# Optimization experiments

Hardware: AMD Instinct MI355X
Metric: run time of the kernel (lower is better)

The kernel has to match this reference:

```python
import jax, jax.numpy as jnp
import numpy as np

HIDDEN = 256
HEADS = 8
HEAD_DIM = HIDDEN // HEADS
NUM_RBF = 32
CUTOFF = 8.0
K_PTS = 4096   # total points (32 molecules x 128)
N_ATOMS = 2048 # total atoms  (32 molecules x 64)
B_MOL = 32


def setup_inputs() -> dict:
    key = jax.random.key(0)
    ks = jax.random.split(key, 12)
    s = 0.02
    return {
        "h_point": jax.random.normal(ks[0], (K_PTS, HIDDEN), jnp.float32),
        "h_atom": jax.random.normal(ks[1], (N_ATOMS, HIDDEN), jnp.float32),
        "pos_point": jax.random.uniform(ks[2], (K_PTS, 3), jnp.float32) * 10.0,
        "pos_atom": jax.random.uniform(ks[3], (N_ATOMS, 3), jnp.float32) * 10.0,
        "Wq": jax.random.normal(ks[4], (HIDDEN, HIDDEN), jnp.float32) * s,
        "bq": jnp.zeros((HIDDEN,), jnp.float32),
        "Wk": jax.random.normal(ks[5], (HIDDEN, HIDDEN), jnp.float32) * s,
        "bk": jnp.zeros((HIDDEN,), jnp.float32),
        "Wv": jax.random.normal(ks[6], (HIDDEN, HIDDEN), jnp.float32) * s,
        "bv": jnp.zeros((HIDDEN,), jnp.float32),
        "Wo": jax.random.normal(ks[7], (HIDDEN, HIDDEN), jnp.float32) * s,
        "bo": jnp.zeros((HIDDEN,), jnp.float32),
        "W_rbf": jax.random.normal(ks[8], (NUM_RBF, HEADS), jnp.float32) * 0.1,
        "b_rbf": jnp.zeros((HEADS,), jnp.float32),
        "centers": jnp.linspace(0.0, CUTOFF, NUM_RBF, dtype=jnp.float32),
        "gamma": jnp.ones((HIDDEN,), jnp.float32),
        "beta": jnp.zeros((HIDDEN,), jnp.float32),
        "point_batch": jnp.repeat(jnp.arange(B_MOL), K_PTS // B_MOL),
        "atom_batch": jnp.repeat(jnp.arange(B_MOL), N_ATOMS // B_MOL),
    }


def reference(h_point, h_atom, pos_point, pos_atom,
              Wq, bq, Wk, bk, Wv, bv, Wo, bo,
              W_rbf, b_rbf, centers, gamma, beta,
              point_batch, atom_batch):
    H, D = HEADS, HEAD_DIM
    Kp = h_point.shape[0]
    Na = h_atom.shape[0]
    scale = D ** -0.5
    width = (CUTOFF / NUM_RBF) ** 2

    q = (h_point @ Wq + bq).reshape(Kp, H, D)
    k = (h_atom @ Wk + bk).reshape(Na, H, D)
    v = (h_atom @ Wv + bv).reshape(Na, H, D)

    # pairwise distances [Kp, Na]
    d2 = jnp.sum((pos_point[:, None, :] - pos_atom[None, :, :]) ** 2, axis=-1)
    dist = jnp.sqrt(jnp.maximum(d2, 0.0))

    # RBF distance bias -> [H, Kp, Na]
    rbf = jnp.exp(-((dist[..., None] - centers) ** 2) / width)  # [Kp, Na, NUM_RBF]
    bias = (rbf @ W_rbf + b_rbf).transpose(2, 0, 1)

    scores = jnp.einsum('khd,nhd->hkn', q, k) * scale + bias
    # ragged structure: point j only attends to atoms in the same molecule
    mask = point_batch[:, None] == atom_batch[None, :]  # [Kp, Na]
    scores = jnp.where(mask[None], scores, -1e30)
    attn = jax.nn.softmax(scores, axis=-1)

    agg = jnp.einsum('hkn,nhd->khd', attn, v).reshape(Kp, H * D)
    agg = agg @ Wo + bo

    x = h_point + agg
    mean = jnp.mean(x, axis=-1, keepdims=True)
    var = jnp.mean((x - mean) ** 2, axis=-1, keepdims=True)
    return (x - mean) * jax.lax.rsqrt(var + 1e-5) * gamma + beta
```

## Files before the change

kernel.cpp:

```cpp
#include <hip/hip_runtime.h>
#include <hip/hip_bf16.h>

#define HIDDEN 256
#define HEADS 8
#define HEAD_DIM 32
#define NUM_RBF 32
#define K_PTS 4096
#define N_ATOMS 2048
#define B_MOL 32
#define ATOMS_PER_MOL (N_ATOMS / B_MOL)

typedef __attribute__((ext_vector_type(8))) short bf16x8;
typedef __attribute__((ext_vector_type(4))) float f32x4;

__global__ __launch_bounds__(256) void prepW_kernel(
    const float* __restrict__ Wq, const float* __restrict__ Wk,
    const float* __restrict__ Wv, const float* __restrict__ Wo,
    __hip_bfloat16* __restrict__ WqT, __hip_bfloat16* __restrict__ WkT,
    __hip_bfloat16* __restrict__ WvT, __hip_bfloat16* __restrict__ WoT) {
    __shared__ float tile[32][33];
    const int t = blockIdx.x, tid = threadIdx.x;
    const int matId = t >> 6, tileId = t & 63;
    const int tr = (tileId >> 3) * 32, tc = (tileId & 7) * 32;
    const float* __restrict__ Ws = (matId == 0) ? Wq : (matId == 1) ? Wk : (matId == 2) ? Wv : Wo;
    __hip_bfloat16* __restrict__ Wd = (matId == 0) ? WqT : (matId == 1) ? WkT : (matId == 2) ? WvT : WoT;

    const int r = tid >> 3, cq = (tid & 7) * 4;
    const float4 in = *(const float4*)&Ws[(size_t)(tr + r) * HIDDEN + tc + cq];
    tile[r][cq + 0] = in.x; tile[r][cq + 1] = in.y;
    tile[r][cq + 2] = in.z; tile[r][cq + 3] = in.w;
    __syncthreads();
    __hip_bfloat16 o[4];
    o[0] = __float2bfloat16(tile[cq + 0][r]);
    o[1] = __float2bfloat16(tile[cq + 1][r]);
    o[2] = __float2bfloat16(tile[cq + 2][r]);
    o[3] = __float2bfloat16(tile[cq + 3][r]);
    *(uint2*)(Wd + (size_t)(tc + r) * HIDDEN + tr + cq) = *(const uint2*)o;
}

__device__ __forceinline__ bf16x8 cvt8(const float* p) {
    const float4 lo = *(const float4*)p;
    const float4 hi = *(const float4*)(p + 4);
    __hip_bfloat16 t[8];
    t[0] = __float2bfloat16(lo.x); t[1] = __float2bfloat16(lo.y);
    t[2] = __float2bfloat16(lo.z); t[3] = __float2bfloat16(lo.w);
    t[4] = __float2bfloat16(hi.x); t[5] = __float2bfloat16(hi.y);
    t[6] = __float2bfloat16(hi.z); t[7] = __float2bfloat16(hi.w);
    return *(const bf16x8*)t;
}

__global__ __launch_bounds__(256) void qkv3_kernel(
    const float* __restrict__ hp, const float* __restrict__ ha,
    const __hip_bfloat16* __restrict__ WqT, const float* __restrict__ bq, __hip_bfloat16* __restrict__ qb,
    const __hip_bfloat16* __restrict__ WkT, const float* __restrict__ bk, __hip_bfloat16* __restrict__ kb,
    const __hip_bfloat16* __restrict__ WvT, const float* __restrict__ bv, __hip_bfloat16* __restrict__ vt) {
    const bool isQ = (blockIdx.x < 256);
    const float* __restrict__ A = isQ ? hp : ha;
    const __hip_bfloat16* __restrict__ W0T = isQ ? WqT : WkT;
    const float* __restrict__ b0 = isQ ? bq : bk;
    const int r0 = (isQ ? blockIdx.x : blockIdx.x - 256) * 16;

    const int wave = threadIdx.x >> 6, lane = threadIdx.x & 63;
    const int c0 = wave * 64;
    const int lrow = lane & 15, kgrp = lane >> 4;

    bf16x8 af[8];
    const float* Arow = A + (size_t)(r0 + lrow) * HIDDEN + kgrp * 8;
#pragma unroll
    for (int ks = 0; ks < 8; ++ks)
        af[ks] = cvt8(Arow + ks * 32);

    f32x4 acc0[4], acc1[4];
#pragma unroll
    for (int cc = 0; cc < 4; ++cc) {
        acc0[cc] = (f32x4){0.f, 0.f, 0.f, 0.f};
        acc1[cc] = (f32x4){0.f, 0.f, 0.f, 0.f};
    }

#pragma unroll
    for (int cc = 0; cc < 4; ++cc) {
        const short* W0r = (const short*)W0T + (size_t)(c0 + cc * 16 + lrow) * HIDDEN + kgrp * 8;
#pragma unroll
        for (int ks = 0; ks < 8; ++ks)
            acc0[cc] = __builtin_amdgcn_mfma_f32_16x16x32_bf16(
                af[ks], *(const bf16x8*)(W0r + ks * 32), acc0[cc], 0, 0, 0);
        if (!isQ) {
            const short* W1r = (const short*)WvT + (size_t)(c0 + cc * 16 + lrow) * HIDDEN + kgrp * 8;
#pragma unroll
            for (int ks = 0; ks < 8; ++ks)
                acc1[cc] = __builtin_amdgcn_mfma_f32_16x16x32_bf16(
                    af[ks], *(const bf16x8*)(W1r + ks * 32), acc1[cc], 0, 0, 0);
        }
    }

    const int colb = lane & 15;
    const int rowb = (lane >> 4) * 4;
#pragma unroll
    for (int cc = 0; cc < 4; ++cc) {
        const int cgl = c0 + cc * 16 + colb;
        const float bias0 = b0[cgl];
        if (isQ) {
#pragma unroll
            for (int rg = 0; rg < 4; ++rg)
                qb[(size_t)(r0 + rowb + rg) * HIDDEN + cgl] = __float2bfloat16(acc0[cc][rg] + bias0);
        } else {
            const float bias1 = bv[cgl];
#pragma unroll
            for (int rg = 0; rg < 4; ++rg) {
                kb[(size_t)(r0 + rowb + rg) * HIDDEN + cgl] = __float2bfloat16(acc0[cc][rg] + bias0);
                vt[(size_t)cgl * N_ATOMS + (r0 + rowb + rg)] = __float2bfloat16(acc1[cc][rg] + bias1);
            }
        }
    }
}

#define AGG_PAD (HIDDEN + 16)

__global__ __launch_bounds__(256) void attn_mfma_kernel(
    const __hip_bfloat16* __restrict__ qb, const __hip_bfloat16* __restrict__ kb,
    const __hip_bfloat16* __restrict__ vt,
    const float* __restrict__ pos_point, const float* __restrict__ pos_atom,
    const float* __restrict__ W_rbf, const float* __restrict__ b_rbf,
    const float* __restrict__ centers,
    const int* __restrict__ point_batch, const int* __restrict__ atom_batch,
    const __hip_bfloat16* __restrict__ WoT, const float* __restrict__ bo,
    const float* __restrict__ h_point,
    const float* __restrict__ gamma, const float* __restrict__ beta,
    float* __restrict__ out) {
    __shared__ float wrbf_lds[NUM_RBF][HEADS];
    __shared__ float cent_lds[NUM_RBF];
    __shared__ float brbf_lds[HEADS];
    __shared__ float bias_lds[HEADS][ATOMS_PER_MOL + 1][8];
    __shared__ __hip_bfloat16 p_lds[HEADS][8][72];
    __shared__ __hip_bfloat16 agg_lds[8][AGG_PAD];
    __shared__ float x_lds[8][260];
    __shared__ float red_s[8][4];
    __shared__ float red_q[8][4];

    const int tid = threadIdx.x, wave = tid >> 6, lane = tid & 63;
    const int j0 = blockIdx.x * 8;
    const float scale = 0.17677669529663687f;

    ((float*)wrbf_lds)[tid] = W_rbf[tid];
    if (tid < NUM_RBF) cent_lds[tid] = centers[tid];
    if (tid < HEADS) brbf_lds[tid] = b_rbf[tid];
    if (tid < 64) {
        bias_lds[tid >> 3][ATOMS_PER_MOL][tid & 7] = 0.0f;
    }
    __syncthreads();

    const int m = point_batch[j0];
    const int mbase = m * ATOMS_PER_MOL;

    {
        const int n = mbase + lane;
        const bool valid = (atom_batch[n] == m);
        const int jA = j0 + wave * 2, jB = jA + 1;

        const float ax = pos_atom[n * 3 + 0], ay = pos_atom[n * 3 + 1], az = pos_atom[n * 3 + 2];
        const float dxA = pos_point[jA * 3 + 0] - ax;
        const float dyA = pos_point[jA * 3 + 1] - ay;
        const float dzA = pos_point[jA * 3 + 2] - az;
        const float dxB = pos_point[jB * 3 + 0] - ax;
        const float dyB = pos_point[jB * 3 + 1] - ay;
        const float dzB = pos_point[jB * 3 + 2] - az;
        const float distA = sqrtf(fmaxf(dxA * dxA + dyA * dyA + dzA * dzA, 0.0f));
        const float distB = sqrtf(fmaxf(dxB * dxB + dyB * dyB + dzB * dzB, 0.0f));

        float biasA[HEADS], biasB[HEADS];
#pragma unroll
        for (int h = 0; h < HEADS; ++h) { biasA[h] = brbf_lds[h]; biasB[h] = brbf_lds[h]; }
#pragma unroll
        for (int r = 0; r < NUM_RBF; ++r) {
            const float cr = cent_lds[r];
            const float ddA = distA - cr, ddB = distB - cr;
            const float eA = __expf(-16.0f * ddA * ddA);
            const float eB = __expf(-16.0f * ddB * ddB);
#pragma unroll
            for (int h = 0; h < HEADS; ++h) {
                const float wr = wrbf_lds[r][h];
                biasA[h] += eA * wr;
                biasB[h] += eB * wr;
            }
        }
#pragma unroll
        for (int h = 0; h < HEADS; ++h) {
            bias_lds[h][lane][wave * 2 + 0] = valid ? biasA[h] : -1e30f;
            bias_lds[h][lane][wave * 2 + 1] = valid ? biasB[h] : -1e30f;
        }
    }
    __syncthreads();

    const int c = lane & 15, kgrp = lane >> 4;
    const int h0 = wave * 2;

#pragma unroll
    for (int hl = 0; hl < 2; ++hl) {
        const int h = h0 + hl;

        const bf16x8 aq = *(const bf16x8*)((const short*)qb +
                          (size_t)(j0 + (c & 7)) * HIDDEN + h * HEAD_DIM + kgrp * 8);

        f32x4 sacc[4];
#pragma unroll
        for (int t = 0; t < 4; ++t) {
            const bf16x8 bk_ = *(const bf16x8*)((const short*)kb +
                               (size_t)(mbase + c + 16 * t) * HIDDEN + h * HEAD_DIM + kgrp * 8);
            sacc[t] = __builtin_amdgcn_mfma_f32_16x16x32_bf16(
                aq, bk_, (f32x4){0.f, 0.f, 0.f, 0.f}, 0, 0, 0);
        }

        float s[4][4];
#pragma unroll
        for (int t = 0; t < 4; ++t) {
            const f32x4 bv = *(const f32x4*)&bias_lds[h][c + 16 * t][kgrp * 4];
#pragma unroll
            for (int r = 0; r < 4; ++r)
                s[t][r] = sacc[t][r] * scale + bv[r];
        }
#pragma unroll
        for (int r = 0; r < 4; ++r) {
            float mx = fmaxf(fmaxf(s[0][r], s[1][r]), fmaxf(s[2][r], s[3][r]));
#pragma unroll
            for (int off = 1; off <= 8; off <<= 1)
                mx = fmaxf(mx, __shfl_xor(mx, off));
            float e0 = __expf(s[0][r] - mx);
            float e1 = __expf(s[1][r] - mx);
            float e2 = __expf(s[2][r] - mx);
            float e3 = __expf(s[3][r] - mx);
            float ss = e0 + e1 + e2 + e3;
#pragma unroll
            for (int off = 1; off <= 8; off <<= 1)
                ss += __shfl_xor(ss, off);
            const float inv = 1.0f / ss;
            if (kgrp < 2) {
                const int pt = kgrp * 4 + r;
                p_lds[h][pt][c + 16 * 0] = __float2bfloat16(e0 * inv);
                p_lds[h][pt][c + 16 * 1] = __float2bfloat16(e1 * inv);
                p_lds[h][pt][c + 16 * 2] = __float2bfloat16(e2 * inv);
                p_lds[h][pt][c + 16 * 3] = __float2bfloat16(e3 * inv);
            }
        }

#pragma unroll
        for (int t2 = 0; t2 < 2; ++t2) {
            f32x4 pacc = (f32x4){0.f, 0.f, 0.f, 0.f};
#pragma unroll
            for (int ks = 0; ks < 2; ++ks) {
                const bf16x8 ap = *(const bf16x8*)&p_lds[h][c & 7][ks * 32 + kgrp * 8];
                const bf16x8 bvv = *(const bf16x8*)((const short*)vt +
                                   (size_t)(h * HEAD_DIM + t2 * 16 + c) * N_ATOMS +
                                   mbase + ks * 32 + kgrp * 8);
                pacc = __builtin_amdgcn_mfma_f32_16x16x32_bf16(ap, bvv, pacc, 0, 0, 0);
            }
            if (kgrp < 2) {
#pragma unroll
                for (int r = 0; r < 4; ++r)
                    agg_lds[kgrp * 4 + r][h * HEAD_DIM + t2 * 16 + c] = __float2bfloat16(pacc[r]);
            }
        }
    }
    __syncthreads();

    const int c0 = wave * 64;
    const int lrow = lane & 15, kgrp2 = lane >> 4;
    bf16x8 af[8];
    const bf16x8 zf = {0, 0, 0, 0, 0, 0, 0, 0};
#pragma unroll
    for (int ks = 0; ks < 8; ++ks)
        af[ks] = (lrow < 8) ? *(const bf16x8*)(&agg_lds[lrow & 7][kgrp2 * 8 + ks * 32]) : zf;

    f32x4 oacc[4];
#pragma unroll
    for (int cc = 0; cc < 4; ++cc) oacc[cc] = (f32x4){0.f, 0.f, 0.f, 0.f};
#pragma unroll
    for (int cc = 0; cc < 4; ++cc) {
        const short* Wr = (const short*)WoT + (size_t)(c0 + cc * 16 + lrow) * HIDDEN + kgrp2 * 8;
#pragma unroll
        for (int ks = 0; ks < 8; ++ks)
            oacc[cc] = __builtin_amdgcn_mfma_f32_16x16x32_bf16(
                af[ks], *(const bf16x8*)(Wr + ks * 32), oacc[cc], 0, 0, 0);
    }

    const int colb = lane & 15;
    const int rowb = (lane >> 4) * 4;
#pragma unroll
    for (int cc = 0; cc < 4; ++cc) {
        const int cgl = c0 + cc * 16 + colb;
        const float bias_o = bo[cgl];
#pragma unroll
        for (int rg = 0; rg < 4; ++rg) {
            const int rl = rowb + rg;
            if (rl < 8)
                x_lds[rl][cgl] = oacc[cc][rg] + bias_o + h_point[(size_t)(j0 + rl) * HIDDEN + cgl];
        }
    }
    __syncthreads();

    const int cc2 = tid;
    const int ln = cc2 & 63, wv = cc2 >> 6;
    float xv[8];
#pragma unroll
    for (int r = 0; r < 8; ++r) {
        xv[r] = x_lds[r][cc2];
        float s = xv[r], qq = xv[r] * xv[r];
#pragma unroll
        for (int off = 32; off > 0; off >>= 1) {
            s += __shfl_xor(s, off);
            qq += __shfl_xor(qq, off);
        }
        if (ln == 0) { red_s[r][wv] = s; red_q[r][wv] = qq; }
    }
    __syncthreads();

    const float gc = gamma[cc2], bc = beta[cc2];
#pragma unroll
    for (int r = 0; r < 8; ++r) {
        const float mean = (red_s[r][0] + red_s[r][1] + red_s[r][2] + red_s[r][3]) * (1.0f / HIDDEN);
        const float ex2  = (red_q[r][0] + red_q[r][1] + red_q[r][2] + red_q[r][3]) * (1.0f / HIDDEN);
        const float var = ex2 - mean * mean;
        out[(size_t)(j0 + r) * HIDDEN + cc2] = (xv[r] - mean) * rsqrtf(var + 1e-5f) * gc + bc;
    }
}

extern "C" void kernel_launch(void* const* d_in, const int* in_sizes, int n_in,
                              void* d_out, int out_size, void* d_ws, size_t ws_size,
                              hipStream_t stream) {
    const float* h_point   = (const float*)d_in[0];
    const float* h_atom    = (const float*)d_in[1];
    const float* pos_point = (const float*)d_in[2];
    const float* pos_atom  = (const float*)d_in[3];
    const float* Wq        = (const float*)d_in[4];
    const float* bq        = (const float*)d_in[5];
    const float* Wk        = (const float*)d_in[6];
    const float* bk        = (const float*)d_in[7];
    const float* Wv        = (const float*)d_in[8];
    const float* bv        = (const float*)d_in[9];
    const float* Wo        = (const float*)d_in[10];
    const float* bo        = (const float*)d_in[11];
    const float* W_rbf     = (const float*)d_in[12];
    const float* b_rbf     = (const float*)d_in[13];
    const float* centers   = (const float*)d_in[14];
    const float* gamma     = (const float*)d_in[15];
    const float* beta      = (const float*)d_in[16];
    const int*   point_batch = (const int*)d_in[17];
    const int*   atom_batch  = (const int*)d_in[18];
    float* out = (float*)d_out;

    __hip_bfloat16* qb = (__hip_bfloat16*)d_ws;
    __hip_bfloat16* kb = qb + (size_t)K_PTS * HIDDEN;
    __hip_bfloat16* vt = kb + (size_t)N_ATOMS * HIDDEN;
    __hip_bfloat16* WqT = vt + (size_t)HIDDEN * N_ATOMS;
    __hip_bfloat16* WkT = WqT + HIDDEN * HIDDEN;
    __hip_bfloat16* WvT = WkT + HIDDEN * HIDDEN;
    __hip_bfloat16* WoT = WvT + HIDDEN * HIDDEN;

    prepW_kernel<<<256, 256, 0, stream>>>(Wq, Wk, Wv, Wo, WqT, WkT, WvT, WoT);

    qkv3_kernel<<<384, 256, 0, stream>>>(h_point, h_atom,
                                         WqT, bq, qb,
                                         WkT, bk, kb,
                                         WvT, bv, vt);

    attn_mfma_kernel<<<K_PTS / 8, 256, 0, stream>>>(qb, kb, vt,
                                                    pos_point, pos_atom,
                                                    W_rbf, b_rbf, centers,
                                                    point_batch, atom_batch,
                                                    WoT, bo, h_point, gamma, beta,
                                                    out);
}
```

Before: 137.1 us.

## Use 8 waves per attention block, one wave per head and point

```diff
diff --git a/kernel.cpp b/kernel.cpp
--- a/kernel.cpp
+++ b/kernel.cpp
@@ -116,7 +116,7 @@
 
 #define AGG_PAD (HIDDEN + 16)
 
-__global__ __launch_bounds__(256) void attn_mfma_kernel(
+__global__ __launch_bounds__(512) void attn_mfma8_kernel(
     const __hip_bfloat16* __restrict__ qb, const __hip_bfloat16* __restrict__ kb,
     const __hip_bfloat16* __restrict__ vt,
     const float* __restrict__ pos_point, const float* __restrict__ pos_atom,
@@ -141,12 +141,10 @@
     const int j0 = blockIdx.x * 8;
     const float scale = 0.17677669529663687f;
 
-    ((float*)wrbf_lds)[tid] = W_rbf[tid];
+    if (tid < NUM_RBF * HEADS) ((float*)wrbf_lds)[tid] = W_rbf[tid];
     if (tid < NUM_RBF) cent_lds[tid] = centers[tid];
     if (tid < HEADS) brbf_lds[tid] = b_rbf[tid];
-    if (tid < 64) {
-        bias_lds[tid >> 3][ATOMS_PER_MOL][tid & 7] = 0.0f;
-    }
+    if (tid < 64) bias_lds[tid >> 3][ATOMS_PER_MOL][tid & 7] = 0.0f;
     __syncthreads();
 
     const int m = point_batch[j0];
@@ -155,49 +153,33 @@
     {
         const int n = mbase + lane;
         const bool valid = (atom_batch[n] == m);
-        const int jA = j0 + wave * 2, jB = jA + 1;
-
-        const float ax = pos_atom[n * 3 + 0], ay = pos_atom[n * 3 + 1], az = pos_atom[n * 3 + 2];
-        const float dxA = pos_point[jA * 3 + 0] - ax;
-        const float dyA = pos_point[jA * 3 + 1] - ay;
-        const float dzA = pos_point[jA * 3 + 2] - az;
-        const float dxB = pos_point[jB * 3 + 0] - ax;
-        const float dyB = pos_point[jB * 3 + 1] - ay;
-        const float dzB = pos_point[jB * 3 + 2] - az;
-        const float distA = sqrtf(fmaxf(dxA * dxA + dyA * dyA + dzA * dzA, 0.0f));
-        const float distB = sqrtf(fmaxf(dxB * dxB + dyB * dyB + dzB * dzB, 0.0f));
-
-        float biasA[HEADS], biasB[HEADS];
-#pragma unroll
-        for (int h = 0; h < HEADS; ++h) { biasA[h] = brbf_lds[h]; biasB[h] = brbf_lds[h]; }
+        const int j = j0 + wave;
+
+        const float dx = pos_point[j * 3 + 0] - pos_atom[n * 3 + 0];
+        const float dy = pos_point[j * 3 + 1] - pos_atom[n * 3 + 1];
+        const float dz = pos_point[j * 3 + 2] - pos_atom[n * 3 + 2];
+        const float dist = sqrtf(fmaxf(dx * dx + dy * dy + dz * dz, 0.0f));
+
+        float bias[HEADS];
+#pragma unroll
+        for (int h = 0; h < HEADS; ++h) bias[h] = brbf_lds[h];
 #pragma unroll
         for (int r = 0; r < NUM_RBF; ++r) {
-            const float cr = cent_lds[r];
-            const float ddA = distA - cr, ddB = distB - cr;
-            const float eA = __expf(-16.0f * ddA * ddA);
-            const float eB = __expf(-16.0f * ddB * ddB);
-#pragma unroll
-            for (int h = 0; h < HEADS; ++h) {
-                const float wr = wrbf_lds[r][h];
-                biasA[h] += eA * wr;
-                biasB[h] += eB * wr;
-            }
-        }
-#pragma unroll
-        for (int h = 0; h < HEADS; ++h) {
-            bias_lds[h][lane][wave * 2 + 0] = valid ? biasA[h] : -1e30f;
-            bias_lds[h][lane][wave * 2 + 1] = valid ? biasB[h] : -1e30f;
-        }
+            const float dd = dist - cent_lds[r];
+            const float e = __expf(-16.0f * dd * dd);
+#pragma unroll
+            for (int h = 0; h < HEADS; ++h)
+                bias[h] += e * wrbf_lds[r][h];
+        }
+#pragma unroll
+        for (int h = 0; h < HEADS; ++h)
+            bias_lds[h][lane][wave] = valid ? bias[h] : -1e30f;
     }
     __syncthreads();
 
     const int c = lane & 15, kgrp = lane >> 4;
-    const int h0 = wave * 2;
-
-#pragma unroll
-    for (int hl = 0; hl < 2; ++hl) {
-        const int h = h0 + hl;
-
+    const int h = wave;
+    {
         const bf16x8 aq = *(const bf16x8*)((const short*)qb +
                           (size_t)(j0 + (c & 7)) * HIDDEN + h * HEAD_DIM + kgrp * 8);
 
@@ -262,7 +244,7 @@
     }
     __syncthreads();
 
-    const int c0 = wave * 64;
+    const int c0 = wave * 32;
     const int lrow = lane & 15, kgrp2 = lane >> 4;
     bf16x8 af[8];
     const bf16x8 zf = {0, 0, 0, 0, 0, 0, 0, 0};
@@ -270,11 +252,11 @@
     for (int ks = 0; ks < 8; ++ks)
         af[ks] = (lrow < 8) ? *(const bf16x8*)(&agg_lds[lrow & 7][kgrp2 * 8 + ks * 32]) : zf;
 
-    f32x4 oacc[4];
-#pragma unroll
-    for (int cc = 0; cc < 4; ++cc) oacc[cc] = (f32x4){0.f, 0.f, 0.f, 0.f};
-#pragma unroll
-    for (int cc = 0; cc < 4; ++cc) {
+    f32x4 oacc[2];
+#pragma unroll
+    for (int cc = 0; cc < 2; ++cc) oacc[cc] = (f32x4){0.f, 0.f, 0.f, 0.f};
+#pragma unroll
+    for (int cc = 0; cc < 2; ++cc) {
         const short* Wr = (const short*)WoT + (size_t)(c0 + cc * 16 + lrow) * HIDDEN + kgrp2 * 8;
 #pragma unroll
         for (int ks = 0; ks < 8; ++ks)
@@ -285,7 +267,7 @@
     const int colb = lane & 15;
     const int rowb = (lane >> 4) * 4;
 #pragma unroll
-    for (int cc = 0; cc < 4; ++cc) {
+    for (int cc = 0; cc < 2; ++cc) {
         const int cgl = c0 + cc * 16 + colb;
         const float bias_o = bo[cgl];
 #pragma unroll
@@ -297,29 +279,32 @@
     }
     __syncthreads();
 
-    const int cc2 = tid;
-    const int ln = cc2 & 63, wv = cc2 >> 6;
-    float xv[8];
-#pragma unroll
-    for (int r = 0; r < 8; ++r) {
-        xv[r] = x_lds[r][cc2];
+    const int col = tid & 255;
+    const int half = tid >> 8;
+    const int ln = col & 63, wv = col >> 6;
+    float xv[4];
+#pragma unroll
+    for (int r = 0; r < 4; ++r) {
+        const int rr = half * 4 + r;
+        xv[r] = x_lds[rr][col];
         float s = xv[r], qq = xv[r] * xv[r];
 #pragma unroll
         for (int off = 32; off > 0; off >>= 1) {
             s += __shfl_xor(s, off);
             qq += __shfl_xor(qq, off);
         }
-        if (ln == 0) { red_s[r][wv] = s; red_q[r][wv] = qq; }
-    }
-    __syncthreads();
-
-    const float gc = gamma[cc2], bc = beta[cc2];
-#pragma unroll
-    for (int r = 0; r < 8; ++r) {
-        const float mean = (red_s[r][0] + red_s[r][1] + red_s[r][2] + red_s[r][3]) * (1.0f / HIDDEN);
-        const float ex2  = (red_q[r][0] + red_q[r][1] + red_q[r][2] + red_q[r][3]) * (1.0f / HIDDEN);
+        if (ln == 0) { red_s[rr][wv] = s; red_q[rr][wv] = qq; }
+    }
+    __syncthreads();
+
+    const float gc = gamma[col], bc = beta[col];
+#pragma unroll
+    for (int r = 0; r < 4; ++r) {
+        const int rr = half * 4 + r;
+        const float mean = (red_s[rr][0] + red_s[rr][1] + red_s[rr][2] + red_s[rr][3]) * (1.0f / HIDDEN);
+        const float ex2  = (red_q[rr][0] + red_q[rr][1] + red_q[rr][2] + red_q[rr][3]) * (1.0f / HIDDEN);
         const float var = ex2 - mean * mean;
-        out[(size_t)(j0 + r) * HIDDEN + cc2] = (xv[r] - mean) * rsqrtf(var + 1e-5f) * gc + bc;
+        out[(size_t)(j0 + rr) * HIDDEN + col] = (xv[r] - mean) * rsqrtf(var + 1e-5f) * gc + bc;
     }
 }
 
@@ -362,10 +347,10 @@
                                          WkT, bk, kb,
                                          WvT, bv, vt);
 
-    attn_mfma_kernel<<<K_PTS / 8, 256, 0, stream>>>(qb, kb, vt,
-                                                    pos_point, pos_atom,
-                                                    W_rbf, b_rbf, centers,
-                                                    point_batch, atom_batch,
-                                                    WoT, bo, h_point, gamma, beta,
-                                                    out);
-}
+    attn_mfma8_kernel<<<K_PTS / 8, 512, 0, stream>>>(qb, kb, vt,
+                                                     pos_point, pos_atom,
+                                                     W_rbf, b_rbf, centers,
+                                                     point_batch, atom_batch,
+                                                     WoT, bo, h_point, gamma, beta,
+                                                     out);
+}
```

Measured after the change: 133.0 us. 3.0% less time.
